# Kernel tuning notes

Hardware: AMD Instinct MI355X
Metric: run time of the kernel (lower is better)

Reference implementation:

```python
import jax, jax.numpy as jnp
import numpy as np

B, S, D, H = 2, 4096, 512, 8
HD = D // H

def setup_inputs() -> dict:
    key = jax.random.key(0)
    ks = jax.random.split(key, 11)
    s = 1.0 / np.sqrt(D)
    return {
        "x": jax.random.normal(ks[0], (B, S, D), jnp.float32),
        "y": jax.random.normal(ks[1], (B, S, D), jnp.float32),
        "z": jax.random.normal(ks[2], (B, S, D), jnp.float32),
        "Wq": jax.random.normal(ks[3], (D, D), jnp.float32) * s,
        "bq": jnp.zeros((D,), jnp.float32),
        "Wk": jax.random.normal(ks[4], (D, D), jnp.float32) * s,
        "bk": jnp.zeros((D,), jnp.float32),
        "Wv": jax.random.normal(ks[5], (D, D), jnp.float32) * s,
        "bv": jnp.zeros((D,), jnp.float32),
        "Wp": jax.random.normal(ks[6], (D, D), jnp.float32) * s,
        "bp": jnp.zeros((D,), jnp.float32),
    }

def reference(x, y, z, Wq, bq, Wk, bk, Wv, bv, Wp, bp):
    # q/k/v projections, split heads: [B,S,D] -> [B,H,S,HD]
    def heads(t):
        return t.reshape(B, -1, H, HD).transpose(0, 2, 1, 3)
    q = heads(x @ Wq + bq)
    k = heads(y @ Wk + bk)
    v = heads(z @ Wv + bv)
    att = jnp.einsum('bhqd,bhkd->bhqk', q, k) / np.sqrt(HD).astype(np.float32)
    att = jax.nn.softmax(att, axis=-1)  # dropout is identity in eval mode
    out = jnp.einsum('bhqk,bhkd->bhqd', att, v)
    out = out.transpose(0, 2, 1, 3).reshape(B, -1, D)
    return out @ Wp + bp
```

## Files before the change

### kernel.cpp

```cpp
#include <hip/hip_runtime.h>
#include <math.h>

#define B_ 2
#define S_ 4096
#define D_ 512
#define H_ 8
#define HD_ 64
#define NROW_ (B_ * S_)
#define NELEM_ ((size_t)NROW_ * D_)
#define WELEM_ ((size_t)D_ * D_)

typedef _Float16 half8 __attribute__((ext_vector_type(8)));
typedef _Float16 half4v __attribute__((ext_vector_type(4)));
typedef _Float16 half2v __attribute__((ext_vector_type(2)));
typedef __fp16 fp16x2 __attribute__((ext_vector_type(2)));
typedef float floatx4 __attribute__((ext_vector_type(4)));

__device__ __forceinline__ half8 cvt_half8(float4 a, float4 b) {
  fp16x2 l0 = __builtin_amdgcn_cvt_pkrtz(a.x, a.y);
  fp16x2 l1 = __builtin_amdgcn_cvt_pkrtz(a.z, a.w);
  fp16x2 l2 = __builtin_amdgcn_cvt_pkrtz(b.x, b.y);
  fp16x2 l3 = __builtin_amdgcn_cvt_pkrtz(b.z, b.w);
  half8 h;
  h[0] = l0[0]; h[1] = l0[1]; h[2] = l1[0]; h[3] = l1[1];
  h[4] = l2[0]; h[5] = l2[1]; h[6] = l3[0]; h[7] = l3[1];
  return h;
}

struct WPtrs { const float *W0, *W1, *W2, *W3; };

__global__ void wT4_kernel(WPtrs p, _Float16* __restrict__ WTbase) {
  __shared__ float tl[32][33];
  const int z = blockIdx.z;
  const float* W = z == 0 ? p.W0 : z == 1 ? p.W1 : z == 2 ? p.W2 : p.W3;
  const float scale = z == 0 ? 0.125f : 1.0f;
  _Float16* Wt = WTbase + (size_t)z * WELEM_;
  const int t = threadIdx.x;
  const int k0 = blockIdx.y * 32, n0 = blockIdx.x * 32;
  const int r = t >> 3, c0 = (t & 7) * 4;
  const float4 v = *(const float4*)&W[(size_t)(k0 + r) * D_ + n0 + c0];
  tl[r][c0 + 0] = v.x; tl[r][c0 + 1] = v.y;
  tl[r][c0 + 2] = v.z; tl[r][c0 + 3] = v.w;
  __syncthreads();
  half4v hv;
#pragma unroll
  for (int j = 0; j < 4; ++j) hv[j] = (_Float16)(tl[c0 + j][r] * scale);
  *(half4v*)&Wt[(size_t)(n0 + r) * D_ + k0 + c0] = hv;
}

__global__ void vT_kernel(const _Float16* __restrict__ Vh,
                          _Float16* __restrict__ VhT) {
  __shared__ alignas(16) _Float16 T[64][72];
  const int t = threadIdx.x;
  const int s0 = blockIdx.x * 64;
  const int h = blockIdx.y, b = blockIdx.z;
  const int srow = t >> 3, soff = (t & 7) * 8;
#pragma unroll
  for (int i = 0; i < 2; ++i)
    *(half8*)&T[srow + 32 * i][soff] = *(const half8*)
        &Vh[(size_t)(b * S_ + s0 + srow + 32 * i) * D_ + h * HD_ + soff];
  __syncthreads();
  const size_t obase = (size_t)(b * H_ + h) * HD_ * S_;
#pragma unroll
  for (int i = 0; i < 2; ++i) {
    half8 o;
#pragma unroll
    for (int j = 0; j < 8; ++j) {
      const int ka = soff + j;
      const int key = 16 * (ka & 3) + (ka >> 2);
      o[j] = T[key][srow + 32 * i];
    }
    *(half8*)&VhT[obase + (size_t)(srow + 32 * i) * S_ + s0 + soff] = o;
  }
}

template <bool AF16, bool OUT16, int BM>
__device__ __forceinline__ void gemm_body(
    const void* __restrict__ Av, const _Float16* __restrict__ Bt,
    const float* __restrict__ bias, void* __restrict__ Cout, float bscale,
    int bx, int by, int tid) {
  constexpr int MT = BM / 32;
  __shared__ alignas(16) _Float16 As[BM][72];
  __shared__ alignas(16) _Float16 Bs[128][72];

  const int w = tid >> 6, lane = tid & 63;
  const int m = lane & 15, quad = lane >> 4;
  const int row0 = by * BM, col0 = bx * 128;
  const int wr = (w >> 1) * (BM / 2), wc = (w & 1) * 64;
  const int srow = tid >> 3, soff = (tid & 7) * 8;

  const _Float16* A16 = (const _Float16*)Av;
  const float* A32 = (const float*)Av;

  floatx4 acc[MT][4];
#pragma unroll
  for (int i = 0; i < MT; ++i)
#pragma unroll
    for (int j = 0; j < 4; ++j) acc[i][j] = floatx4{0.f, 0.f, 0.f, 0.f};

  half8 pa16[MT];
  float4 pa32[MT][2];
  half8 pb[4];
#pragma unroll
  for (int i = 0; i < MT; ++i) {
    const size_t ar = (size_t)(row0 + srow + 32 * i) * D_ + soff;
    if (AF16) pa16[i] = *(const half8*)&A16[ar];
    else { pa32[i][0] = *(const float4*)&A32[ar];
           pa32[i][1] = *(const float4*)&A32[ar + 4]; }
  }
#pragma unroll
  for (int i = 0; i < 4; ++i)
    pb[i] = *(const half8*)&Bt[(size_t)(col0 + srow + 32 * i) * D_ + soff];

  for (int kt = 0; kt < D_ / 64; ++kt) {
    if (kt) __syncthreads();
#pragma unroll
    for (int i = 0; i < MT; ++i)
      *(half8*)&As[srow + 32 * i][soff] =
          AF16 ? pa16[i] : cvt_half8(pa32[i][0], pa32[i][1]);
#pragma unroll
    for (int i = 0; i < 4; ++i) *(half8*)&Bs[srow + 32 * i][soff] = pb[i];
    __syncthreads();
    if (kt < D_ / 64 - 1) {
      const int kc = (kt + 1) * 64 + soff;
#pragma unroll
      for (int i = 0; i < MT; ++i) {
        const size_t ar = (size_t)(row0 + srow + 32 * i) * D_ + kc;
        if (AF16) pa16[i] = *(const half8*)&A16[ar];
        else { pa32[i][0] = *(const float4*)&A32[ar];
               pa32[i][1] = *(const float4*)&A32[ar + 4]; }
      }
#pragma unroll
      for (int i = 0; i < 4; ++i)
        pb[i] = *(const half8*)&Bt[(size_t)(col0 + srow + 32 * i) * D_ + kc];
    }
#pragma unroll
    for (int h = 0; h < 2; ++h) {
      half8 af[MT], bf[4];
#pragma unroll
      for (int mt = 0; mt < MT; ++mt)
        af[mt] = *(const half8*)&As[wr + mt * 16 + m][h * 32 + quad * 8];
#pragma unroll
      for (int nt = 0; nt < 4; ++nt)
        bf[nt] = *(const half8*)&Bs[wc + nt * 16 + m][h * 32 + quad * 8];
#pragma unroll
      for (int mt = 0; mt < MT; ++mt)
#pragma unroll
        for (int nt = 0; nt < 4; ++nt)
          acc[mt][nt] = __builtin_amdgcn_mfma_f32_16x16x32_f16(
              af[mt], bf[nt], acc[mt][nt], 0, 0, 0);
    }
  }

  float bv[4];
#pragma unroll
  for (int nt = 0; nt < 4; ++nt)
    bv[nt] = bias[col0 + wc + nt * 16 + m] * bscale;
#pragma unroll
  for (int mt = 0; mt < MT; ++mt)
#pragma unroll
    for (int nt = 0; nt < 4; ++nt)
#pragma unroll
      for (int r = 0; r < 4; ++r) {
        const int row = row0 + wr + mt * 16 + quad * 4 + r;
        const int col = col0 + wc + nt * 16 + m;
        const float vout = acc[mt][nt][r] + bv[nt];
        if (OUT16)
          ((_Float16*)Cout)[(size_t)row * D_ + col] = (_Float16)vout;
        else
          ((float*)Cout)[(size_t)row * D_ + col] = vout;
      }
}

struct QkvPtrs { const float *A0, *A1, *A2, *b0, *b1, *b2; };

__global__ __launch_bounds__(256, 3) void qkv_gemm_kernel(
    QkvPtrs p, const _Float16* __restrict__ WT, _Float16* __restrict__ Cb) {
  const int z = blockIdx.z;
  const float* A = z == 0 ? p.A0 : z == 1 ? p.A1 : p.A2;
  const float* bias = z == 0 ? p.b0 : z == 1 ? p.b1 : p.b2;
  gemm_body<false, true, 128>(A, WT + (size_t)z * WELEM_, bias,
                              Cb + (size_t)z * NELEM_, z == 0 ? 0.125f : 1.0f,
                              blockIdx.x, blockIdx.y, threadIdx.x);
}

__global__ __launch_bounds__(256, 2) void out_gemm_kernel(
    const _Float16* __restrict__ Oh, const _Float16* __restrict__ WpT,
    const float* __restrict__ bp, float* __restrict__ out) {
  gemm_body<true, false, 64>(Oh, WpT, bp, out, 1.0f, blockIdx.x, blockIdx.y,
                             threadIdx.x);
}

__global__ __launch_bounds__(512, 4) void attn_mfma_kernel(
    const _Float16* __restrict__ Qg, const _Float16* __restrict__ Kg,
    const _Float16* __restrict__ VT, _Float16* __restrict__ Og) {
  __shared__ alignas(16) _Float16 Ks[2][64][72];
  __shared__ alignas(16) _Float16 Vt[2][64][72];
  __shared__ alignas(16) _Float16 Ps[128][72];

  const int t = threadIdx.x;
  const int w = t >> 6;
  const int lane = t & 63;
  const int m = lane & 15;
  const int quad = lane >> 4;
  const int q0 = blockIdx.x * 128;
  const size_t base =
      (size_t)blockIdx.z * ((size_t)S_ * D_) + (size_t)blockIdx.y * HD_;
  const size_t vbase = (size_t)(blockIdx.z * H_ + blockIdx.y) * HD_ * S_;

  half8 qf[2];
#pragma unroll
  for (int h = 0; h < 2; ++h)
    qf[h] = *(const half8*)
        &Qg[base + (size_t)(q0 + w * 16 + m) * D_ + h * 32 + quad * 8];

  floatx4 oacc[4];
  float lpart[4];
#pragma unroll
  for (int n = 0; n < 4; ++n) oacc[n] = floatx4{0.f, 0.f, 0.f, 0.f};
#pragma unroll
  for (int r = 0; r < 4; ++r) lpart[r] = 0.f;

  const int srow = t >> 3;
  const int soff = (t & 7) * 8;

  half8 pk = *(const half8*)&Kg[base + (size_t)srow * D_ + soff];
  half8 pv = *(const half8*)&VT[vbase + (size_t)srow * S_ + soff];
  *(half8*)&Ks[0][srow][soff] = pk;
  *(half8*)&Vt[0][srow][soff] = pv;
  pk = *(const half8*)&Kg[base + (size_t)(64 + srow) * D_ + soff];
  pv = *(const half8*)&VT[vbase + (size_t)srow * S_ + 64 + soff];
  __syncthreads();

  constexpr int NT = S_ / 64;
  for (int kt = 0; kt < NT; ++kt) {
    const int cur = kt & 1;
    if (kt + 1 < NT) {
      *(half8*)&Ks[cur ^ 1][srow][soff] = pk;
      *(half8*)&Vt[cur ^ 1][srow][soff] = pv;
      if (kt + 2 < NT) {
        const int k2 = (kt + 2) * 64;
        pk = *(const half8*)&Kg[base + (size_t)(k2 + srow) * D_ + soff];
        pv = *(const half8*)&VT[vbase + (size_t)srow * S_ + k2 + soff];
      }
    }

    floatx4 sacc[4];
#pragma unroll
    for (int n = 0; n < 4; ++n) sacc[n] = floatx4{0.f, 0.f, 0.f, 0.f};
    __builtin_amdgcn_s_setprio(1);
#pragma unroll
    for (int n = 0; n < 4; ++n)
#pragma unroll
      for (int h = 0; h < 2; ++h) {
        const half8 bf =
            *(const half8*)&Ks[cur][n * 16 + m][h * 32 + quad * 8];
        sacc[n] = __builtin_amdgcn_mfma_f32_16x16x32_f16(
            qf[h], bf, sacc[n], 0, 0, 0);
      }
    __builtin_amdgcn_s_setprio(0);

    const int prow = w * 16 + quad * 4;
#pragma unroll
    for (int r = 0; r < 4; ++r) {
      const float p0 = __expf(fminf(sacc[0][r], 11.f));
      const float p1 = __expf(fminf(sacc[1][r], 11.f));
      const float p2 = __expf(fminf(sacc[2][r], 11.f));
      const float p3 = __expf(fminf(sacc[3][r], 11.f));
      lpart[r] += (p0 + p1) + (p2 + p3);
      const fp16x2 plo = __builtin_amdgcn_cvt_pkrtz(p0, p1);
      const fp16x2 phi = __builtin_amdgcn_cvt_pkrtz(p2, p3);
      half4v ph;
      ph[0] = plo[0]; ph[1] = plo[1]; ph[2] = phi[0]; ph[3] = phi[1];
      *(half4v*)&Ps[prow + r][4 * m] = ph;
    }

    const half8 af0 = *(const half8*)&Ps[w * 16 + m][quad * 8];
    const half8 af1 = *(const half8*)&Ps[w * 16 + m][32 + quad * 8];
    __builtin_amdgcn_s_setprio(1);
#pragma unroll
    for (int n = 0; n < 4; ++n) {
      const half8 b0 = *(const half8*)&Vt[cur][n * 16 + m][quad * 8];
      const half8 b1 = *(const half8*)&Vt[cur][n * 16 + m][32 + quad * 8];
      oacc[n] = __builtin_amdgcn_mfma_f32_16x16x32_f16(
          af0, b0, oacc[n], 0, 0, 0);
      oacc[n] = __builtin_amdgcn_mfma_f32_16x16x32_f16(
          af1, b1, oacc[n], 0, 0, 0);
    }
    __builtin_amdgcn_s_setprio(0);

    __syncthreads();
  }

  float linv[4];
#pragma unroll
  for (int r = 0; r < 4; ++r) {
    float ls = lpart[r];
    ls += __shfl_xor(ls, 1);
    ls += __shfl_xor(ls, 2);
    ls += __shfl_xor(ls, 4);
    ls += __shfl_xor(ls, 8);
    linv[r] = 1.0f / ls;
  }
#pragma unroll
  for (int n = 0; n < 4; ++n)
#pragma unroll
    for (int r = 0; r < 4; ++r)
      Og[base + (size_t)(q0 + w * 16 + quad * 4 + r) * D_ + n * 16 + m] =
          (_Float16)(oacc[n][r] * linv[r]);
}

extern "C" void kernel_launch(void* const* d_in, const int* in_sizes, int n_in,
                              void* d_out, int out_size, void* d_ws,
                              size_t ws_size, hipStream_t stream) {
  const float* x  = (const float*)d_in[0];
  const float* y  = (const float*)d_in[1];
  const float* z  = (const float*)d_in[2];
  const float* Wq = (const float*)d_in[3];
  const float* bq = (const float*)d_in[4];
  const float* Wk = (const float*)d_in[5];
  const float* bk = (const float*)d_in[6];
  const float* Wv = (const float*)d_in[7];
  const float* bv = (const float*)d_in[8];
  const float* Wp = (const float*)d_in[9];
  const float* bp = (const float*)d_in[10];

  _Float16* hws = (_Float16*)d_ws;
  _Float16* WT  = hws;
  _Float16* Qh  = WT + 4 * WELEM_;
  _Float16* Kh  = Qh + NELEM_;
  _Float16* Vh  = Kh + NELEM_;
  _Float16* Oh  = Vh + NELEM_;
  _Float16* VhT = Oh + NELEM_;

  WPtrs wp{Wq, Wk, Wv, Wp};
  wT4_kernel<<<dim3(16, 16, 4), 256, 0, stream>>>(wp, WT);

  QkvPtrs qp{x, y, z, bq, bk, bv};
  qkv_gemm_kernel<<<dim3(4, 64, 3), 256, 0, stream>>>(qp, WT, Qh);

  vT_kernel<<<dim3(S_ / 64, H_, B_), 256, 0, stream>>>(Vh, VhT);

  attn_mfma_kernel<<<dim3(S_ / 128, H_, B_), 512, 0, stream>>>(Qh, Kh, VhT, Oh);

  out_gemm_kernel<<<dim3(4, 128), 256, 0, stream>>>(Oh, WT + 3 * WELEM_, bp,
                                                    (float*)d_out);
}
```

Before: 258.7 us.

## Switch attention to 32x32x16 MFMA with register-resident P via permlane32 swap

Rewrites the attention kernel to compute S^T = K·Q^T with 32x32x16 MFMAs, four waves of 32 queries each, so the softmax probabilities stay in registers. A permlane32 swap rearranges them into the B-operand layout for the PV MFMA, which removes the Ps shared-memory round trip. The V transpose kernel drops its key permutation to match. Blocks shrink to 256 threads with more work per wave, which lowers occupancy and adds register pressure from the 16-wide accumulators.

```diff
diff --git a/kernel.cpp b/kernel.cpp
--- a/kernel.cpp
+++ b/kernel.cpp
@@ -15,6 +15,9 @@
 typedef _Float16 half2v __attribute__((ext_vector_type(2)));
 typedef __fp16 fp16x2 __attribute__((ext_vector_type(2)));
 typedef float floatx4 __attribute__((ext_vector_type(4)));
+typedef float floatx16 __attribute__((ext_vector_type(16)));
+typedef int intx2 __attribute__((ext_vector_type(2)));
+typedef unsigned uintx4 __attribute__((ext_vector_type(4)));
 
 __device__ __forceinline__ half8 cvt_half8(float4 a, float4 b) {
   fp16x2 l0 = __builtin_amdgcn_cvt_pkrtz(a.x, a.y);
@@ -25,6 +28,16 @@
   h[0] = l0[0]; h[1] = l0[1]; h[2] = l1[0]; h[3] = l1[1];
   h[4] = l2[0]; h[5] = l2[1]; h[6] = l3[0]; h[7] = l3[1];
   return h;
+}
+
+__device__ __forceinline__ void permswap32(unsigned& a, unsigned& b) {
+#if __has_builtin(__builtin_amdgcn_permlane32_swap)
+  intx2 r = __builtin_amdgcn_permlane32_swap((int)a, (int)b, false, false);
+  a = (unsigned)r[0];
+  b = (unsigned)r[1];
+#else
+  asm volatile("v_permlane32_swap_b32 %0, %1" : "+v"(a), "+v"(b));
+#endif
 }
 
 struct WPtrs { const float *W0, *W1, *W2, *W3; };
@@ -65,11 +78,7 @@
   for (int i = 0; i < 2; ++i) {
     half8 o;
 #pragma unroll
-    for (int j = 0; j < 8; ++j) {
-      const int ka = soff + j;
-      const int key = 16 * (ka & 3) + (ka >> 2);
-      o[j] = T[key][srow + 32 * i];
-    }
+    for (int j = 0; j < 8; ++j) o[j] = T[soff + j][srow + 32 * i];
     *(half8*)&VhT[obase + (size_t)(srow + 32 * i) * S_ + s0 + soff] = o;
   }
 }
@@ -191,123 +200,140 @@
                              threadIdx.x);
 }
 
-__global__ __launch_bounds__(512, 4) void attn_mfma_kernel(
+__global__ __launch_bounds__(256, 2) void attn_mfma_kernel(
     const _Float16* __restrict__ Qg, const _Float16* __restrict__ Kg,
     const _Float16* __restrict__ VT, _Float16* __restrict__ Og) {
   __shared__ alignas(16) _Float16 Ks[2][64][72];
   __shared__ alignas(16) _Float16 Vt[2][64][72];
-  __shared__ alignas(16) _Float16 Ps[128][72];
 
   const int t = threadIdx.x;
   const int w = t >> 6;
   const int lane = t & 63;
-  const int m = lane & 15;
-  const int quad = lane >> 4;
-  const int q0 = blockIdx.x * 128;
+  const int li = lane & 31;
+  const int hl = lane >> 5;
+  const int q0 = blockIdx.x * 128 + w * 32;
   const size_t base =
       (size_t)blockIdx.z * ((size_t)S_ * D_) + (size_t)blockIdx.y * HD_;
   const size_t vbase = (size_t)(blockIdx.z * H_ + blockIdx.y) * HD_ * S_;
 
-  half8 qf[2];
-#pragma unroll
-  for (int h = 0; h < 2; ++h)
-    qf[h] = *(const half8*)
-        &Qg[base + (size_t)(q0 + w * 16 + m) * D_ + h * 32 + quad * 8];
-
-  floatx4 oacc[4];
-  float lpart[4];
-#pragma unroll
-  for (int n = 0; n < 4; ++n) oacc[n] = floatx4{0.f, 0.f, 0.f, 0.f};
-#pragma unroll
-  for (int r = 0; r < 4; ++r) lpart[r] = 0.f;
-
-  const int srow = t >> 3;
-  const int soff = (t & 7) * 8;
-
-  half8 pk = *(const half8*)&Kg[base + (size_t)srow * D_ + soff];
-  half8 pv = *(const half8*)&VT[vbase + (size_t)srow * S_ + soff];
-  *(half8*)&Ks[0][srow][soff] = pk;
-  *(half8*)&Vt[0][srow][soff] = pv;
-  pk = *(const half8*)&Kg[base + (size_t)(64 + srow) * D_ + soff];
-  pv = *(const half8*)&VT[vbase + (size_t)srow * S_ + 64 + soff];
+  half8 qb[4];
+#pragma unroll
+  for (int ks = 0; ks < 4; ++ks)
+    qb[ks] = *(const half8*)
+        &Qg[base + (size_t)(q0 + li) * D_ + ks * 16 + hl * 8];
+
+  floatx16 oacc[2];
+#pragma unroll
+  for (int i = 0; i < 16; ++i) { oacc[0][i] = 0.f; oacc[1][i] = 0.f; }
+  float lpart = 0.f;
+
+  const int srow = t >> 3, soff = (t & 7) * 8;
+
+#pragma unroll
+  for (int i = 0; i < 2; ++i) {
+    *(half8*)&Ks[0][srow + 32 * i][soff] =
+        *(const half8*)&Kg[base + (size_t)(srow + 32 * i) * D_ + soff];
+    *(half8*)&Vt[0][srow + 32 * i][soff] =
+        *(const half8*)&VT[vbase + (size_t)(srow + 32 * i) * S_ + soff];
+  }
+  half8 pk[2], pv[2];
+#pragma unroll
+  for (int i = 0; i < 2; ++i) {
+    pk[i] = *(const half8*)&Kg[base + (size_t)(64 + srow + 32 * i) * D_ + soff];
+    pv[i] = *(const half8*)&VT[vbase + (size_t)(srow + 32 * i) * S_ + 64 + soff];
+  }
   __syncthreads();
 
   constexpr int NT = S_ / 64;
   for (int kt = 0; kt < NT; ++kt) {
     const int cur = kt & 1;
     if (kt + 1 < NT) {
-      *(half8*)&Ks[cur ^ 1][srow][soff] = pk;
-      *(half8*)&Vt[cur ^ 1][srow][soff] = pv;
+#pragma unroll
+      for (int i = 0; i < 2; ++i) {
+        *(half8*)&Ks[cur ^ 1][srow + 32 * i][soff] = pk[i];
+        *(half8*)&Vt[cur ^ 1][srow + 32 * i][soff] = pv[i];
+      }
       if (kt + 2 < NT) {
         const int k2 = (kt + 2) * 64;
-        pk = *(const half8*)&Kg[base + (size_t)(k2 + srow) * D_ + soff];
-        pv = *(const half8*)&VT[vbase + (size_t)srow * S_ + k2 + soff];
-      }
-    }
-
-    floatx4 sacc[4];
-#pragma unroll
-    for (int n = 0; n < 4; ++n) sacc[n] = floatx4{0.f, 0.f, 0.f, 0.f};
+#pragma unroll
+        for (int i = 0; i < 2; ++i) {
+          pk[i] = *(const half8*)
+              &Kg[base + (size_t)(k2 + srow + 32 * i) * D_ + soff];
+          pv[i] = *(const half8*)
+              &VT[vbase + (size_t)(srow + 32 * i) * S_ + k2 + soff];
+        }
+      }
+    }
+
+    floatx16 sacc[2];
+#pragma unroll
+    for (int i = 0; i < 16; ++i) { sacc[0][i] = 0.f; sacc[1][i] = 0.f; }
     __builtin_amdgcn_s_setprio(1);
 #pragma unroll
-    for (int n = 0; n < 4; ++n)
-#pragma unroll
-      for (int h = 0; h < 2; ++h) {
-        const half8 bf =
-            *(const half8*)&Ks[cur][n * 16 + m][h * 32 + quad * 8];
-        sacc[n] = __builtin_amdgcn_mfma_f32_16x16x32_f16(
-            qf[h], bf, sacc[n], 0, 0, 0);
-      }
+    for (int ks = 0; ks < 4; ++ks) {
+      const half8 ka0 = *(const half8*)&Ks[cur][li][ks * 16 + hl * 8];
+      const half8 ka1 = *(const half8*)&Ks[cur][32 + li][ks * 16 + hl * 8];
+      sacc[0] = __builtin_amdgcn_mfma_f32_32x32x16_f16(ka0, qb[ks],
+                                                       sacc[0], 0, 0, 0);
+      sacc[1] = __builtin_amdgcn_mfma_f32_32x32x16_f16(ka1, qb[ks],
+                                                       sacc[1], 0, 0, 0);
+    }
     __builtin_amdgcn_s_setprio(0);
 
-    const int prow = w * 16 + quad * 4;
-#pragma unroll
-    for (int r = 0; r < 4; ++r) {
-      const float p0 = __expf(fminf(sacc[0][r], 11.f));
-      const float p1 = __expf(fminf(sacc[1][r], 11.f));
-      const float p2 = __expf(fminf(sacc[2][r], 11.f));
-      const float p3 = __expf(fminf(sacc[3][r], 11.f));
-      lpart[r] += (p0 + p1) + (p2 + p3);
-      const fp16x2 plo = __builtin_amdgcn_cvt_pkrtz(p0, p1);
-      const fp16x2 phi = __builtin_amdgcn_cvt_pkrtz(p2, p3);
-      half4v ph;
-      ph[0] = plo[0]; ph[1] = plo[1]; ph[2] = phi[0]; ph[3] = phi[1];
-      *(half4v*)&Ps[prow + r][4 * m] = ph;
-    }
-
-    const half8 af0 = *(const half8*)&Ps[w * 16 + m][quad * 8];
-    const half8 af1 = *(const half8*)&Ps[w * 16 + m][32 + quad * 8];
+    half8 pfrag[4];
+#pragma unroll
+    for (int kt2 = 0; kt2 < 2; ++kt2) {
+      unsigned dq[4][2];
+#pragma unroll
+      for (int rq = 0; rq < 4; ++rq)
+#pragma unroll
+        for (int pp = 0; pp < 2; ++pp) {
+          const float e0 = __expf(fminf(sacc[kt2][4 * rq + 2 * pp], 11.f));
+          const float e1 = __expf(fminf(sacc[kt2][4 * rq + 2 * pp + 1], 11.f));
+          lpart += e0 + e1;
+          const fp16x2 h2 = __builtin_amdgcn_cvt_pkrtz(e0, e1);
+          dq[rq][pp] = __builtin_bit_cast(unsigned, h2);
+        }
+#pragma unroll
+      for (int t2 = 0; t2 < 2; ++t2) {
+        unsigned a0 = dq[2 * t2][0], b0 = dq[2 * t2 + 1][0];
+        unsigned a1 = dq[2 * t2][1], b1 = dq[2 * t2 + 1][1];
+        permswap32(a0, b0);
+        permswap32(a1, b1);
+        uintx4 u; u[0] = a0; u[1] = a1; u[2] = b0; u[3] = b1;
+        pfrag[2 * kt2 + t2] = __builtin_bit_cast(half8, u);
+      }
+    }
+
     __builtin_amdgcn_s_setprio(1);
 #pragma unroll
-    for (int n = 0; n < 4; ++n) {
-      const half8 b0 = *(const half8*)&Vt[cur][n * 16 + m][quad * 8];
-      const half8 b1 = *(const half8*)&Vt[cur][n * 16 + m][32 + quad * 8];
-      oacc[n] = __builtin_amdgcn_mfma_f32_16x16x32_f16(
-          af0, b0, oacc[n], 0, 0, 0);
-      oacc[n] = __builtin_amdgcn_mfma_f32_16x16x32_f16(
-          af1, b1, oacc[n], 0, 0, 0);
+    for (int ks = 0; ks < 4; ++ks) {
+      const half8 va0 = *(const half8*)&Vt[cur][li][ks * 16 + hl * 8];
+      const half8 va1 = *(const half8*)&Vt[cur][32 + li][ks * 16 + hl * 8];
+      oacc[0] = __builtin_amdgcn_mfma_f32_32x32x16_f16(va0, pfrag[ks],
+                                                       oacc[0], 0, 0, 0);
+      oacc[1] = __builtin_amdgcn_mfma_f32_32x32x16_f16(va1, pfrag[ks],
+                                                       oacc[1], 0, 0, 0);
     }
     __builtin_amdgcn_s_setprio(0);
 
     __syncthreads();
   }
 
-  float linv[4];
-#pragma unroll
-  for (int r = 0; r < 4; ++r) {
-    float ls = lpart[r];
-    ls += __shfl_xor(ls, 1);
-    ls += __shfl_xor(ls, 2);
-    ls += __shfl_xor(ls, 4);
-    ls += __shfl_xor(ls, 8);
-    linv[r] = 1.0f / ls;
-  }
-#pragma unroll
-  for (int n = 0; n < 4; ++n)
-#pragma unroll
-    for (int r = 0; r < 4; ++r)
-      Og[base + (size_t)(q0 + w * 16 + quad * 4 + r) * D_ + n * 16 + m] =
-          (_Float16)(oacc[n][r] * linv[r]);
+  const float lsum = lpart + __shfl_xor(lpart, 32);
+  const float linv = 1.0f / lsum;
+
+#pragma unroll
+  for (int n = 0; n < 2; ++n)
+#pragma unroll
+    for (int rq = 0; rq < 4; ++rq) {
+      half4v o4;
+#pragma unroll
+      for (int bb = 0; bb < 4; ++bb)
+        o4[bb] = (_Float16)(oacc[n][4 * rq + bb] * linv);
+      *(half4v*)&Og[base + (size_t)(q0 + li) * D_ +
+                    n * 32 + 8 * rq + 4 * hl] = o4;
+    }
 }
 
 extern "C" void kernel_launch(void* const* d_in, const int* in_sizes, int n_in,
@@ -341,7 +367,7 @@
 
   vT_kernel<<<dim3(S_ / 64, H_, B_), 256, 0, stream>>>(Vh, VhT);
 
-  attn_mfma_kernel<<<dim3(S_ / 128, H_, B_), 512, 0, stream>>>(Qh, Kh, VhT, Oh);
+  attn_mfma_kernel<<<dim3(S_ / 128, H_, B_), 256, 0, stream>>>(Qh, Kh, VhT, Oh);
 
   out_gemm_kernel<<<dim3(4, 128), 256, 0, stream>>>(Oh, WT + 3 * WELEM_, bp,
                                                     (float*)d_out);
```

New measurement: 256.9 us. About the same (-0.7%).
